# Optimization experiments

Hardware: AMD Instinct MI355X
Metric: run time of the kernel (lower is better)

The kernel has to match this reference:

```python
import jax, jax.numpy as jnp
import numpy as np

B, S, E = 32, 1024, 512   # batch, source length, encoder/decoder/attn dim
D, U = 512, 512


def setup_inputs() -> dict:
    key = jax.random.key(0)
    k1, k2, k3, k4, k5 = jax.random.split(key, 5)
    return {
        "outp_enc": jax.random.normal(k1, (B, S, E), dtype=jnp.float32),
        "hidden_dec": jax.random.normal(k2, (B, D), dtype=jnp.float32),
        "Wa": jax.random.normal(k3, (D, U), dtype=jnp.float32) * (1.0 / np.sqrt(D)),
        "Ua": jax.random.normal(k4, (E, U), dtype=jnp.float32) * (1.0 / np.sqrt(E)),
        "Va": jax.random.normal(k5, (U,), dtype=jnp.float32) * (1.0 / np.sqrt(U)),
    }


def reference(outp_enc, hidden_dec, Wa, Ua, Va):
    # Additive (Bahdanau) attention.
    # energies: tanh(Wa h_dec + Ua enc_s) -> [B, S, U]
    dec_proj = hidden_dec @ Wa                      # [B, U]
    enc_proj = jnp.einsum("bse,eu->bsu", outp_enc, Ua)  # [B, S, U]
    e = jnp.tanh(enc_proj + dec_proj[:, None, :])   # [B, S, U]
    scores = jnp.einsum("bsu,u->bs", e, Va)          # [B, S]
    alpha = jax.nn.softmax(scores, axis=-1)          # [B, S]
    context = jnp.einsum("bs,bse->be", alpha, outp_enc)  # [B, E]
    return context
```

## Files before the change

kernel.cpp:

```cpp
#include <hip/hip_runtime.h>
#include <cstdint>
#include <cstddef>

#define BB 32
#define SS 1024
#define EE 512
#define UU 512
#define DD 512

typedef unsigned short ushort_t;
typedef __attribute__((ext_vector_type(8))) short s16x8;
typedef __attribute__((ext_vector_type(4))) float f32x4;

#define AS1(p) ((const __attribute__((address_space(1))) void*)(const void*)(p))
#define AS3(p) ((__attribute__((address_space(3))) void*)(void*)(p))

__device__ inline ushort_t bf16_rn(float x, float& hi_f) {
    uint32_t u = __float_as_uint(x);
    uint32_t r = (u + 0x7FFFu + ((u >> 16) & 1u)) >> 16;
    hi_f = __uint_as_float(r << 16);
    return (ushort_t)r;
}

__device__ inline float fast_tanh(float x) {
    float ax = fminf(fabsf(x), 20.0f);
    float e2 = __expf(ax * 2.0f);
    float t  = 1.0f - __fdividef(2.0f, e2 + 1.0f);
    return (x < 0.0f) ? -t : t;
}

__global__ void prep_kernel(const float* __restrict__ Ua,
                            const float* __restrict__ hid,
                            const float* __restrict__ Wa,
                            ushort_t* __restrict__ UaSwz,
                            float* __restrict__ decp) {
    __shared__ float sm[256];
    int blk = blockIdx.x, t = threadIdx.x;
    if (blk < 128) {
        int g    = blk * 256 + t;
        int tile = g >> 10;
        int c    = g & 1023;
        int nt = tile >> 3, kt = tile & 7;
        int n = c >> 3, kp = c & 7;
        int ko = kp ^ (n & 7);
        int u  = nt * 128 + n;
        int e0 = kt * 64 + ko * 8;
        s16x8 v;
#pragma unroll
        for (int j = 0; j < 8; ++j) {
            float hf;
            v[j] = (short)bf16_rn(Ua[(size_t)(e0 + j) * UU + u], hf);
        }
        *(s16x8*)(UaSwz + (size_t)g * 8) = v;
    } else {
        int q2 = blk - 128;
        int b = q2 >> 3, q = q2 & 7;
        int uo = t & 63, ch = t >> 6;
        const float* h = hid + (size_t)b * DD;
        float a = 0.f;
        int d0 = ch * 128;
#pragma unroll 4
        for (int d = d0; d < d0 + 128; ++d)
            a = fmaf(h[d], Wa[(size_t)d * UU + q * 64 + uo], a);
        sm[t] = a;
        __syncthreads();
        if (t < 64) {
            float s = sm[t] + sm[64 + t] + sm[128 + t] + sm[192 + t];
            decp[(size_t)b * UU + q * 64 + t] = s;
        }
    }
}

__global__ __launch_bounds__(256, 2)
void scores_kernel(const float* __restrict__ enc,
                   const ushort_t* __restrict__ UaSwz,
                   const float* __restrict__ decp,
                   const float* __restrict__ Va,
                   float* __restrict__ scores) {
    __shared__ __align__(16) ushort_t lds_b[2][128 * 64];
    __shared__ float lds_dv[1024];

    const int tid  = threadIdx.x;
    const int lane = tid & 63;
    const int wave = tid >> 6;
    const int bid  = blockIdx.x;
    const int b    = bid >> 4;
    const int s0   = (bid & 15) * 64;

    lds_dv[tid]       = decp[(size_t)b * UU + tid];
    lds_dv[256 + tid] = decp[(size_t)b * UU + 256 + tid];
    lds_dv[512 + tid] = Va[tid];
    lds_dv[768 + tid] = Va[256 + tid];

    const float* A = enc + ((size_t)b * SS + s0 + wave * 16 + (lane & 15)) * EE
                         + ((lane >> 4) * 8);
    s16x8 a_hi[16], a_lo[16];
#pragma unroll
    for (int ks = 0; ks < 16; ++ks) {
        f32x4 v0 = *(const f32x4*)(A + ks * 32);
        f32x4 v1 = *(const f32x4*)(A + ks * 32 + 4);
        s16x8 sh, sl;
#pragma unroll
        for (int j = 0; j < 4; ++j) {
            float hf, d;
            sh[j]     = (short)bf16_rn(v0[j], hf);
            sl[j]     = (short)bf16_rn(v0[j] - hf, d);
            sh[4 + j] = (short)bf16_rn(v1[j], hf);
            sl[4 + j] = (short)bf16_rn(v1[j] - hf, d);
        }
        a_hi[ks] = sh;
        a_lo[ks] = sl;
    }
    __syncthreads();

    const int nl  = lane & 15;
    const int kq  = lane >> 4;
    const int l7  = lane & 7;
    const int rb  = nl * 64;
    const int kp0 = ((0 + kq) ^ l7) * 8;
    const int kp1 = ((4 + kq) ^ l7) * 8;

#define STAGE(tile, par)                                                        \
    {                                                                           \
        _Pragma("unroll")                                                       \
        for (int i = 0; i < 4; ++i) {                                           \
            __builtin_amdgcn_global_load_lds(                                   \
                AS1(UaSwz + (size_t)(tile) * 8192 +                             \
                    (((wave * 4 + i) * 64 + lane) * 8)),                        \
                AS3(&lds_b[par][(wave * 4 + i) * 512]), 16, 0, 0);              \
        }                                                                       \
    }

    float sp0 = 0.f, sp1 = 0.f, sp2 = 0.f, sp3 = 0.f;

    STAGE(0, 0);

#pragma unroll 1
    for (int nt = 0; nt < 4; ++nt) {
        f32x4 acc[8];
#pragma unroll
        for (int nf = 0; nf < 8; ++nf) acc[nf] = f32x4{0.f, 0.f, 0.f, 0.f};

#pragma unroll
        for (int kt = 0; kt < 8; ++kt) {
            int t = nt * 8 + kt;
            int nxt = (t < 31) ? (t + 1) : 0;
            STAGE(nxt, (kt + 1) & 1);
            asm volatile("s_waitcnt vmcnt(4)" ::: "memory");
            __builtin_amdgcn_s_barrier();

            const ushort_t* bp = lds_b[kt & 1];
#pragma unroll
            for (int ks = 0; ks < 2; ++ks) {
                const int kpo = ks ? kp1 : kp0;
#pragma unroll
                for (int nf = 0; nf < 8; ++nf) {
                    s16x8 bh = *(const s16x8*)(bp + nf * 1024 + rb + kpo);
                    acc[nf] = __builtin_amdgcn_mfma_f32_16x16x32_bf16(
                        a_hi[kt * 2 + ks], bh, acc[nf], 0, 0, 0);
                    acc[nf] = __builtin_amdgcn_mfma_f32_16x16x32_bf16(
                        a_lo[kt * 2 + ks], bh, acc[nf], 0, 0, 0);
                }
            }
            asm volatile("s_waitcnt lgkmcnt(0)" ::: "memory");
            __builtin_amdgcn_s_barrier();
        }

#pragma unroll
        for (int nf = 0; nf < 8; ++nf) {
            int n = nt * 128 + nf * 16 + nl;
            float dp = lds_dv[n];
            float va = lds_dv[512 + n];
            sp0 += fast_tanh(acc[nf][0] + dp) * va;
            sp1 += fast_tanh(acc[nf][1] + dp) * va;
            sp2 += fast_tanh(acc[nf][2] + dp) * va;
            sp3 += fast_tanh(acc[nf][3] + dp) * va;
        }
    }
    asm volatile("s_waitcnt vmcnt(0)" ::: "memory");

#pragma unroll
    for (int off = 1; off < 16; off <<= 1) {
        sp0 += __shfl_xor(sp0, off, 64);
        sp1 += __shfl_xor(sp1, off, 64);
        sp2 += __shfl_xor(sp2, off, 64);
        sp3 += __shfl_xor(sp3, off, 64);
    }
    if (nl == 0) {
        int m = kq * 4;
        float* o = scores + (size_t)b * SS + s0 + wave * 16 + m;
        o[0] = sp0; o[1] = sp1; o[2] = sp2; o[3] = sp3;
    }
#undef STAGE
}

__global__ void context_partial(const float* __restrict__ enc,
                                const float* __restrict__ sc,
                                float* __restrict__ part) {
    __shared__ float red[8];
    __shared__ float al[128];
    int bid = blockIdx.x;
    int b = bid >> 3, scn = bid & 7;
    int t = threadIdx.x, lane = t & 63, wave = t >> 6;

    f32x4 v = *(const f32x4*)(sc + (size_t)b * SS + t * 4);
    float m = fmaxf(fmaxf(v[0], v[1]), fmaxf(v[2], v[3]));
#pragma unroll
    for (int off = 1; off < 64; off <<= 1) m = fmaxf(m, __shfl_xor(m, off, 64));
    if (lane == 0) red[wave] = m;
    __syncthreads();
    m = fmaxf(fmaxf(red[0], red[1]), fmaxf(red[2], red[3]));

    float e0 = __expf(v[0] - m), e1 = __expf(v[1] - m);
    float e2 = __expf(v[2] - m), e3 = __expf(v[3] - m);
    float s = e0 + e1 + e2 + e3;
#pragma unroll
    for (int off = 1; off < 64; off <<= 1) s += __shfl_xor(s, off, 64);
    if (lane == 0) red[4 + wave] = s;
    __syncthreads();
    s = red[4] + red[5] + red[6] + red[7];
    float inv = 1.0f / s;

    int base = scn * 32;
    if (t >= base && t < base + 32) {
        int i0 = (t - base) * 4;
        al[i0 + 0] = e0 * inv; al[i0 + 1] = e1 * inv;
        al[i0 + 2] = e2 * inv; al[i0 + 3] = e3 * inv;
    }
    __syncthreads();

    const float* basep = enc + ((size_t)b * SS + scn * 128) * EE;
    float a0 = 0.f, a1 = 0.f;
#pragma unroll 4
    for (int si = 0; si < 128; ++si) {
        float w = al[si];
        a0 = fmaf(w, basep[(size_t)si * EE + t], a0);
        a1 = fmaf(w, basep[(size_t)si * EE + t + 256], a1);
    }
    float* p = part + ((size_t)scn * BB + b) * EE;
    p[t] = a0;
    p[t + 256] = a1;
}

__global__ void context_reduce(const float* __restrict__ part,
                               float* __restrict__ out) {
    int g = blockIdx.x * 256 + threadIdx.x;
    float s = 0.f;
#pragma unroll
    for (int scn = 0; scn < 8; ++scn) s += part[(size_t)scn * BB * EE + g];
    out[g] = s;
}

extern "C" void kernel_launch(void* const* d_in, const int* in_sizes, int n_in,
                              void* d_out, int out_size, void* d_ws, size_t ws_size,
                              hipStream_t stream) {
    const float* enc = (const float*)d_in[0];
    const float* hid = (const float*)d_in[1];
    const float* Wa  = (const float*)d_in[2];
    const float* Ua  = (const float*)d_in[3];
    const float* Va  = (const float*)d_in[4];
    float* out = (float*)d_out;

    char* ws = (char*)d_ws;
    float*    decp   = (float*)(ws);
    float*    scores = (float*)(ws + 65536);
    float*    part   = (float*)(ws + 196608);
    ushort_t* UaSwz  = (ushort_t*)(ws + 720896);

    prep_kernel<<<384, 256, 0, stream>>>(Ua, hid, Wa, UaSwz, decp);
    scores_kernel<<<BB * 16, 256, 0, stream>>>(enc, UaSwz, decp, Va, scores);
    context_partial<<<BB * 8, 256, 0, stream>>>(enc, scores, part);
    context_reduce<<<64, 256, 0, stream>>>(part, out);
}
```

Baseline: 80.96 us.

## Split scores GEMM over U halves and double context_partial block count

```diff
diff --git a/kernel.cpp b/kernel.cpp
--- a/kernel.cpp
+++ b/kernel.cpp
@@ -71,26 +71,27 @@
     }
 }
 
-__global__ __launch_bounds__(256, 2)
+__global__ __launch_bounds__(256, 4)
 void scores_kernel(const float* __restrict__ enc,
                    const ushort_t* __restrict__ UaSwz,
                    const float* __restrict__ decp,
                    const float* __restrict__ Va,
-                   float* __restrict__ scores) {
+                   float* __restrict__ scpart) {
     __shared__ __align__(16) ushort_t lds_b[2][128 * 64];
-    __shared__ float lds_dv[1024];
+    __shared__ float lds_dv[512];
 
     const int tid  = threadIdx.x;
     const int lane = tid & 63;
     const int wave = tid >> 6;
-    const int bid  = blockIdx.x;
-    const int b    = bid >> 4;
-    const int s0   = (bid & 15) * 64;
-
-    lds_dv[tid]       = decp[(size_t)b * UU + tid];
-    lds_dv[256 + tid] = decp[(size_t)b * UU + 256 + tid];
-    lds_dv[512 + tid] = Va[tid];
-    lds_dv[768 + tid] = Va[256 + tid];
+    const int p  = blockIdx.x;
+    const int L  = (p & 7) * 128 + (p >> 3);
+    const int uh = L & 1;
+    const int st = (L >> 1) & 15;
+    const int b  = L >> 5;
+    const int s0 = st * 64;
+
+    lds_dv[tid]       = decp[(size_t)b * UU + uh * 256 + tid];
+    lds_dv[256 + tid] = Va[uh * 256 + tid];
 
     const float* A = enc + ((size_t)b * SS + s0 + wave * 16 + (lane & 15)) * EE
                          + ((lane >> 4) * 8);
@@ -132,24 +133,25 @@
     }
 
     float sp0 = 0.f, sp1 = 0.f, sp2 = 0.f, sp3 = 0.f;
-
-    STAGE(0, 0);
+    const int tbase = uh * 16;
+
+    STAGE(tbase, 0);
 
 #pragma unroll 1
-    for (int nt = 0; nt < 4; ++nt) {
+    for (int pass = 0; pass < 2; ++pass) {
         f32x4 acc[8];
 #pragma unroll
         for (int nf = 0; nf < 8; ++nf) acc[nf] = f32x4{0.f, 0.f, 0.f, 0.f};
 
 #pragma unroll
         for (int kt = 0; kt < 8; ++kt) {
-            int t = nt * 8 + kt;
-            int nxt = (t < 31) ? (t + 1) : 0;
-            STAGE(nxt, (kt + 1) & 1);
+            int t8  = pass * 8 + kt;
+            int nxt = (t8 < 15) ? (t8 + 1) : 0;
+            STAGE(tbase + nxt, (t8 + 1) & 1);
             asm volatile("s_waitcnt vmcnt(4)" ::: "memory");
             __builtin_amdgcn_s_barrier();
 
-            const ushort_t* bp = lds_b[kt & 1];
+            const ushort_t* bp = lds_b[t8 & 1];
 #pragma unroll
             for (int ks = 0; ks < 2; ++ks) {
                 const int kpo = ks ? kp1 : kp0;
@@ -168,9 +170,9 @@
 
 #pragma unroll
         for (int nf = 0; nf < 8; ++nf) {
-            int n = nt * 128 + nf * 16 + nl;
+            int n = pass * 128 + nf * 16 + nl;
             float dp = lds_dv[n];
-            float va = lds_dv[512 + n];
+            float va = lds_dv[256 + n];
             sp0 += fast_tanh(acc[nf][0] + dp) * va;
             sp1 += fast_tanh(acc[nf][1] + dp) * va;
             sp2 += fast_tanh(acc[nf][2] + dp) * va;
@@ -188,22 +190,25 @@
     }
     if (nl == 0) {
         int m = kq * 4;
-        float* o = scores + (size_t)b * SS + s0 + wave * 16 + m;
+        float* o = scpart + (size_t)uh * BB * SS + (size_t)b * SS + s0 + wave * 16 + m;
         o[0] = sp0; o[1] = sp1; o[2] = sp2; o[3] = sp3;
     }
 #undef STAGE
 }
 
 __global__ void context_partial(const float* __restrict__ enc,
-                                const float* __restrict__ sc,
+                                const float* __restrict__ scp,
                                 float* __restrict__ part) {
     __shared__ float red[8];
-    __shared__ float al[128];
+    __shared__ float al[64];
     int bid = blockIdx.x;
-    int b = bid >> 3, scn = bid & 7;
+    int b = bid >> 4, scn = bid & 15;
     int t = threadIdx.x, lane = t & 63, wave = t >> 6;
 
-    f32x4 v = *(const f32x4*)(sc + (size_t)b * SS + t * 4);
+    f32x4 v0 = *(const f32x4*)(scp + (size_t)b * SS + t * 4);
+    f32x4 v1 = *(const f32x4*)(scp + (size_t)BB * SS + (size_t)b * SS + t * 4);
+    f32x4 v = {v0[0] + v1[0], v0[1] + v1[1], v0[2] + v1[2], v0[3] + v1[3]};
+
     float m = fmaxf(fmaxf(v[0], v[1]), fmaxf(v[2], v[3]));
 #pragma unroll
     for (int off = 1; off < 64; off <<= 1) m = fmaxf(m, __shfl_xor(m, off, 64));
@@ -221,25 +226,24 @@
     s = red[4] + red[5] + red[6] + red[7];
     float inv = 1.0f / s;
 
-    int base = scn * 32;
-    if (t >= base && t < base + 32) {
-        int i0 = (t - base) * 4;
+    if (t >= scn * 16 && t < scn * 16 + 16) {
+        int i0 = (t - scn * 16) * 4;
         al[i0 + 0] = e0 * inv; al[i0 + 1] = e1 * inv;
         al[i0 + 2] = e2 * inv; al[i0 + 3] = e3 * inv;
     }
     __syncthreads();
 
-    const float* basep = enc + ((size_t)b * SS + scn * 128) * EE;
+    const float* basep = enc + ((size_t)b * SS + scn * 64) * EE;
     float a0 = 0.f, a1 = 0.f;
 #pragma unroll 4
-    for (int si = 0; si < 128; ++si) {
+    for (int si = 0; si < 64; ++si) {
         float w = al[si];
         a0 = fmaf(w, basep[(size_t)si * EE + t], a0);
         a1 = fmaf(w, basep[(size_t)si * EE + t + 256], a1);
     }
-    float* p = part + ((size_t)scn * BB + b) * EE;
-    p[t] = a0;
-    p[t + 256] = a1;
+    float* pp = part + ((size_t)scn * BB + b) * EE;
+    pp[t] = a0;
+    pp[t + 256] = a1;
 }
 
 __global__ void context_reduce(const float* __restrict__ part,
@@ -247,7 +251,7 @@
     int g = blockIdx.x * 256 + threadIdx.x;
     float s = 0.f;
 #pragma unroll
-    for (int scn = 0; scn < 8; ++scn) s += part[(size_t)scn * BB * EE + g];
+    for (int scn = 0; scn < 16; ++scn) s += part[(size_t)scn * BB * EE + g];
     out[g] = s;
 }
 
@@ -263,12 +267,12 @@
 
     char* ws = (char*)d_ws;
     float*    decp   = (float*)(ws);
-    float*    scores = (float*)(ws + 65536);
-    float*    part   = (float*)(ws + 196608);
-    ushort_t* UaSwz  = (ushort_t*)(ws + 720896);
+    float*    scpart = (float*)(ws + 65536);
+    float*    part   = (float*)(ws + 327680);
+    ushort_t* UaSwz  = (ushort_t*)(ws + 1376256);
 
     prep_kernel<<<384, 256, 0, stream>>>(Ua, hid, Wa, UaSwz, decp);
-    scores_kernel<<<BB * 16, 256, 0, stream>>>(enc, UaSwz, decp, Va, scores);
-    context_partial<<<BB * 8, 256, 0, stream>>>(enc, scores, part);
+    scores_kernel<<<1024, 256, 0, stream>>>(enc, UaSwz, decp, Va, scpart);
+    context_partial<<<512, 256, 0, stream>>>(enc, scpart, part);
     context_reduce<<<64, 256, 0, stream>>>(part, out);
 }
```

New measurement: 196.3 us. +142.5%, slower.
